# Performance work log

Measured on AMD Instinct MI355X. Metric: run time of the kernel, lower is better.

## Reference

```python
import jax, jax.numpy as jnp
import numpy as np

B, N, D = 32, 2048, 128
SQRT_DIM = np.sqrt(float(D)).astype(np.float32)  # scale=True -> 1/sqrt(dim)
MASK_FILL = -65504.0  # value used by masked_fill_ in the torch module


def setup_inputs() -> dict:
    key = jax.random.key(0)
    kq, kk, kv = jax.random.split(key, 3)
    return {
        "query": jax.random.normal(kq, (B, N, D), dtype=jnp.float32),
        "key": jax.random.normal(kk, (B, N, D), dtype=jnp.float32),
        "value": jax.random.normal(kv, (B, N, D), dtype=jnp.float32),
        "mask": jnp.ones((B, N, N), dtype=bool),
    }


def reference(query, key, value, mask):
    # score = Q K^T / sqrt(d)   -> [B, N, N]
    score = jnp.einsum("bnd,bmd->bnm", query, key) / SQRT_DIM
    # masked_fill_(~mask, -65504)
    score = jnp.where(mask, score, MASK_FILL)
    attn = jax.nn.softmax(score, axis=-1)
    # context = attn @ V        -> [B, N, D]
    context = jnp.einsum("bnm,bmd->bnd", attn, value)
    return (context, attn)
```

## Files before the change

### kernel.cpp

```cpp
#include <hip/hip_runtime.h>
#include <stdint.h>

#define B_ 32
#define N_ 2048
#define D_ 128
#define TQ 16
#define NW 8
#define CPW (N_ / NW)
#define NT (CPW / 16)
#define SCALE 0.08838834764831845f
#define MASK_FILL -65504.0f

typedef __attribute__((ext_vector_type(8))) short short8;
typedef __attribute__((ext_vector_type(4))) float f32x4;
typedef __attribute__((ext_vector_type(4))) int i32x4;

static __device__ __forceinline__ short f2bf(float f) {
    unsigned u = __builtin_bit_cast(unsigned, f);
    u += 0x7FFFu + ((u >> 16) & 1u);
    return (short)(u >> 16);
}

__global__ __launch_bounds__(512, 4)
void attn_fused_kernel(const float* __restrict__ Q, const float* __restrict__ K,
                       const float* __restrict__ V, const int* __restrict__ mask,
                       float* __restrict__ attn, float* __restrict__ ctx) {
    extern __shared__ char smem[];
    char*  Pb   = smem;
    float* redm = (float*)(smem + TQ * N_ * 2);
    float* reds = redm + NW * TQ;

    int wg = blockIdx.x;
    wg = (wg & 7) * (4096 / 8) + (wg >> 3);
    const int b    = wg >> 7;
    const int row0 = (wg & 127) * TQ;

    const int tid  = threadIdx.x;
    const int w    = tid >> 6;
    const int lane = tid & 63;
    const int l16  = lane & 15;
    const int quad = lane >> 4;

    const size_t qkvbase = (size_t)b * N_ * D_;

    short8 qf[4];
    {
        const float* qp = Q + qkvbase + (size_t)(row0 + l16) * D_ + quad * 8;
        #pragma unroll
        for (int kt = 0; kt < 4; ++kt) {
            f32x4 x = *(const f32x4*)(qp + kt * 32);
            f32x4 y = *(const f32x4*)(qp + kt * 32 + 4);
            #pragma unroll
            for (int j = 0; j < 4; ++j) { qf[kt][j] = f2bf(x[j]); qf[kt][4 + j] = f2bf(y[j]); }
        }
    }

    const int* mrow = mask + ((size_t)b * N_ + row0 + l16) * N_ + w * CPW + quad * 4;
    f32x4 acc[NT];
    float mmax = -INFINITY;
    #pragma unroll
    for (int t = 0; t < NT; ++t) {
        const int c0 = w * CPW + t * 16;
        const float* kp = K + qkvbase + (size_t)(c0 + l16) * D_ + quad * 8;
        i32x4 mv = *(const i32x4*)(mrow + t * 16);
        f32x4 a = {0.f, 0.f, 0.f, 0.f};
        #pragma unroll
        for (int kt = 0; kt < 4; ++kt) {
            f32x4 x = *(const f32x4*)(kp + kt * 32);
            f32x4 y = *(const f32x4*)(kp + kt * 32 + 4);
            short8 kf;
            #pragma unroll
            for (int j = 0; j < 4; ++j) { kf[j] = f2bf(x[j]); kf[4 + j] = f2bf(y[j]); }
            a = __builtin_amdgcn_mfma_f32_16x16x32_bf16(kf, qf[kt], a, 0, 0, 0);
        }
        #pragma unroll
        for (int r = 0; r < 4; ++r) {
            float s = mv[r] ? a[r] * SCALE : MASK_FILL;
            a[r] = s;
            mmax = fmaxf(mmax, s);
        }
        acc[t] = a;
    }

    mmax = fmaxf(mmax, __shfl_xor(mmax, 16));
    mmax = fmaxf(mmax, __shfl_xor(mmax, 32));
    if (quad == 0) redm[w * TQ + l16] = mmax;
    __syncthreads();
    float m = redm[l16];
    #pragma unroll
    for (int w2 = 1; w2 < NW; ++w2) m = fmaxf(m, redm[w2 * TQ + l16]);

    float sum = 0.f;
    #pragma unroll
    for (int t = 0; t < NT; ++t) {
        #pragma unroll
        for (int r = 0; r < 4; ++r) {
            float e = __expf(acc[t][r] - m);
            acc[t][r] = e;
            sum += e;
        }
    }
    sum += __shfl_xor(sum, 16);
    sum += __shfl_xor(sum, 32);
    if (quad == 0) reds[w * TQ + l16] = sum;
    __syncthreads();
    float rsum = reds[l16];
    #pragma unroll
    for (int w2 = 1; w2 < NW; ++w2) rsum += reds[w2 * TQ + l16];
    const float inv = 1.f / rsum;

    float* arow = attn + ((size_t)b * N_ + row0 + l16) * N_ + w * CPW + quad * 4;
    const unsigned pbase = (unsigned)(l16 * (N_ * 2) + (w * CPW + quad * 4) * 2);
    const unsigned swz   = (unsigned)((l16 & 7) << 4);
    #pragma unroll
    for (int t = 0; t < NT; ++t) {
        f32x4 vout;
        #pragma unroll
        for (int r = 0; r < 4; ++r) vout[r] = acc[t][r] * inv;
        *(f32x4*)(arow + t * 16) = vout;
        unsigned lo = (unsigned)(unsigned short)f2bf(vout[0]) | ((unsigned)(unsigned short)f2bf(vout[1]) << 16);
        unsigned hi = (unsigned)(unsigned short)f2bf(vout[2]) | ((unsigned)(unsigned short)f2bf(vout[3]) << 16);
        *(unsigned long long*)(Pb + ((pbase + t * 32) ^ swz)) = ((unsigned long long)hi << 32) | lo;
    }
    __syncthreads();

    const int n0 = w * 16;
    f32x4 o = {0.f, 0.f, 0.f, 0.f};
    const unsigned prbase = (unsigned)(l16 * (N_ * 2) + quad * 16);
    const float* vcol = V + qkvbase + (size_t)(quad * 8) * D_ + n0 + l16;
    #pragma unroll 4
    for (int kk = 0; kk < N_; kk += 32) {
        short8 pf = *(const short8*)(Pb + ((prbase + kk * 2) ^ swz));
        short8 vf;
        #pragma unroll
        for (int j = 0; j < 8; ++j) vf[j] = f2bf(vcol[(size_t)(kk + j) * D_]);
        o = __builtin_amdgcn_mfma_f32_16x16x32_bf16(vf, pf, o, 0, 0, 0);
    }
    float* crow = ctx + ((size_t)b * N_ + row0 + l16) * D_ + n0 + quad * 4;
    *(f32x4*)crow = o;
}

extern "C" void kernel_launch(void* const* d_in, const int* in_sizes, int n_in,
                              void* d_out, int out_size, void* d_ws, size_t ws_size,
                              hipStream_t stream) {
    const float* Q    = (const float*)d_in[0];
    const float* K    = (const float*)d_in[1];
    const float* V    = (const float*)d_in[2];
    const int*   mask = (const int*)d_in[3];

    float* out  = (float*)d_out;
    float* ctx  = out;
    float* attn = out + (size_t)B_ * N_ * D_;

    dim3 grid(B_ * (N_ / TQ), 1, 1);
    dim3 block(512, 1, 1);
    const size_t lds = (size_t)TQ * N_ * 2 + 2 * NW * TQ * sizeof(float);

    attn_fused_kernel<<<grid, block, lds, stream>>>(Q, K, V, mask, attn, ctx);
}
```

Measured before the change: 1.527 ms.

## Pre-convert K to bf16 and V to transposed bf16 in workspace

Adds two pre-pass kernels that convert K to bf16 and write V as a transposed bf16 copy into the workspace. The fused attention kernel can then load ready-made bf16 fragments with contiguous vector loads instead of converting fp32 inside the kernel and gathering V with strided scalar loads. Other changes: nontemporal loads for the mask, nontemporal stores for attn and ctx, and two accumulators in the PV loop. The cost is two extra launches and extra workspace traffic, and it falls back to the old path when the workspace is too small.

```diff
diff --git a/kernel.cpp b/kernel.cpp
--- a/kernel.cpp
+++ b/kernel.cpp
@@ -14,6 +14,8 @@
 typedef __attribute__((ext_vector_type(8))) short short8;
 typedef __attribute__((ext_vector_type(4))) float f32x4;
 typedef __attribute__((ext_vector_type(4))) int i32x4;
+typedef __attribute__((ext_vector_type(4))) unsigned short ushort4_t;
+typedef unsigned short ushort_t;
 
 static __device__ __forceinline__ short f2bf(float f) {
     unsigned u = __builtin_bit_cast(unsigned, f);
@@ -21,9 +23,41 @@
     return (short)(u >> 16);
 }
 
+__global__ __launch_bounds__(256)
+void conv_bf16_kernel(const float* __restrict__ X, ushort_t* __restrict__ Y) {
+    const size_t i = ((size_t)blockIdx.x * 256 + threadIdx.x) * 8;
+    f32x4 a = *(const f32x4*)(X + i);
+    f32x4 c = *(const f32x4*)(X + i + 4);
+    short8 o;
+    #pragma unroll
+    for (int j = 0; j < 4; ++j) { o[j] = f2bf(a[j]); o[4 + j] = f2bf(c[j]); }
+    *(short8*)(Y + i) = o;
+}
+
+__global__ __launch_bounds__(256)
+void conv_vt_kernel(const float* __restrict__ V, ushort_t* __restrict__ Vt) {
+    __shared__ ushort_t t[32][34];
+    const int tid = threadIdx.x;
+    const int b = blockIdx.z, n0 = blockIdx.x * 32, d0 = blockIdx.y * 32;
+    {
+        const int r = tid >> 3, cg = (tid & 7) * 4;
+        f32x4 v = *(const f32x4*)(V + ((size_t)b * N_ + n0 + r) * D_ + d0 + cg);
+        #pragma unroll
+        for (int j = 0; j < 4; ++j) t[r][cg + j] = (ushort_t)f2bf(v[j]);
+    }
+    __syncthreads();
+    {
+        const int d = tid >> 3, ng = (tid & 7) * 4;
+        ushort4_t o = { t[ng][d], t[ng + 1][d], t[ng + 2][d], t[ng + 3][d] };
+        *(ushort4_t*)(Vt + ((size_t)b * D_ + d0 + d) * N_ + n0 + ng) = o;
+    }
+}
+
+template <int PRE>
 __global__ __launch_bounds__(512, 4)
 void attn_fused_kernel(const float* __restrict__ Q, const float* __restrict__ K,
-                       const float* __restrict__ V, const int* __restrict__ mask,
+                       const ushort_t* __restrict__ Kb, const float* __restrict__ V,
+                       const ushort_t* __restrict__ Vt, const int* __restrict__ mask,
                        float* __restrict__ attn, float* __restrict__ ctx) {
     extern __shared__ char smem[];
     char*  Pb   = smem;
@@ -61,17 +95,26 @@
     #pragma unroll
     for (int t = 0; t < NT; ++t) {
         const int c0 = w * CPW + t * 16;
-        const float* kp = K + qkvbase + (size_t)(c0 + l16) * D_ + quad * 8;
-        i32x4 mv = *(const i32x4*)(mrow + t * 16);
+        i32x4 mv = __builtin_nontemporal_load((const i32x4*)(mrow + t * 16));
         f32x4 a = {0.f, 0.f, 0.f, 0.f};
-        #pragma unroll
-        for (int kt = 0; kt < 4; ++kt) {
-            f32x4 x = *(const f32x4*)(kp + kt * 32);
-            f32x4 y = *(const f32x4*)(kp + kt * 32 + 4);
-            short8 kf;
-            #pragma unroll
-            for (int j = 0; j < 4; ++j) { kf[j] = f2bf(x[j]); kf[4 + j] = f2bf(y[j]); }
-            a = __builtin_amdgcn_mfma_f32_16x16x32_bf16(kf, qf[kt], a, 0, 0, 0);
+        if constexpr (PRE) {
+            const ushort_t* kp = Kb + qkvbase + (size_t)(c0 + l16) * D_ + quad * 8;
+            #pragma unroll
+            for (int kt = 0; kt < 4; ++kt) {
+                short8 kf = *(const short8*)(kp + kt * 32);
+                a = __builtin_amdgcn_mfma_f32_16x16x32_bf16(kf, qf[kt], a, 0, 0, 0);
+            }
+        } else {
+            const float* kp = K + qkvbase + (size_t)(c0 + l16) * D_ + quad * 8;
+            #pragma unroll
+            for (int kt = 0; kt < 4; ++kt) {
+                f32x4 x = *(const f32x4*)(kp + kt * 32);
+                f32x4 y = *(const f32x4*)(kp + kt * 32 + 4);
+                short8 kf;
+                #pragma unroll
+                for (int j = 0; j < 4; ++j) { kf[j] = f2bf(x[j]); kf[4 + j] = f2bf(y[j]); }
+                a = __builtin_amdgcn_mfma_f32_16x16x32_bf16(kf, qf[kt], a, 0, 0, 0);
+            }
         }
         #pragma unroll
         for (int r = 0; r < 4; ++r) {
@@ -117,7 +160,7 @@
         f32x4 vout;
         #pragma unroll
         for (int r = 0; r < 4; ++r) vout[r] = acc[t][r] * inv;
-        *(f32x4*)(arow + t * 16) = vout;
+        __builtin_nontemporal_store(vout, (f32x4*)(arow + t * 16));
         unsigned lo = (unsigned)(unsigned short)f2bf(vout[0]) | ((unsigned)(unsigned short)f2bf(vout[1]) << 16);
         unsigned hi = (unsigned)(unsigned short)f2bf(vout[2]) | ((unsigned)(unsigned short)f2bf(vout[3]) << 16);
         *(unsigned long long*)(Pb + ((pbase + t * 32) ^ swz)) = ((unsigned long long)hi << 32) | lo;
@@ -125,19 +168,39 @@
     __syncthreads();
 
     const int n0 = w * 16;
-    f32x4 o = {0.f, 0.f, 0.f, 0.f};
+    f32x4 o0 = {0.f, 0.f, 0.f, 0.f};
+    f32x4 o1 = {0.f, 0.f, 0.f, 0.f};
     const unsigned prbase = (unsigned)(l16 * (N_ * 2) + quad * 16);
-    const float* vcol = V + qkvbase + (size_t)(quad * 8) * D_ + n0 + l16;
-    #pragma unroll 4
-    for (int kk = 0; kk < N_; kk += 32) {
-        short8 pf = *(const short8*)(Pb + ((prbase + kk * 2) ^ swz));
-        short8 vf;
-        #pragma unroll
-        for (int j = 0; j < 8; ++j) vf[j] = f2bf(vcol[(size_t)(kk + j) * D_]);
-        o = __builtin_amdgcn_mfma_f32_16x16x32_bf16(vf, pf, o, 0, 0, 0);
-    }
+    if constexpr (PRE) {
+        const ushort_t* vrow = Vt + qkvbase + (size_t)(n0 + l16) * N_ + quad * 8;
+        #pragma unroll 2
+        for (int kk = 0; kk < N_; kk += 64) {
+            short8 pf0 = *(const short8*)(Pb + ((prbase + kk * 2) ^ swz));
+            short8 pf1 = *(const short8*)(Pb + ((prbase + kk * 2 + 64) ^ swz));
+            short8 vf0 = *(const short8*)(vrow + kk);
+            short8 vf1 = *(const short8*)(vrow + kk + 32);
+            o0 = __builtin_amdgcn_mfma_f32_16x16x32_bf16(vf0, pf0, o0, 0, 0, 0);
+            o1 = __builtin_amdgcn_mfma_f32_16x16x32_bf16(vf1, pf1, o1, 0, 0, 0);
+        }
+    } else {
+        const float* vcol = V + qkvbase + (size_t)(quad * 8) * D_ + n0 + l16;
+        #pragma unroll 2
+        for (int kk = 0; kk < N_; kk += 64) {
+            short8 pf0 = *(const short8*)(Pb + ((prbase + kk * 2) ^ swz));
+            short8 pf1 = *(const short8*)(Pb + ((prbase + kk * 2 + 64) ^ swz));
+            short8 vf0, vf1;
+            #pragma unroll
+            for (int j = 0; j < 8; ++j) {
+                vf0[j] = f2bf(vcol[(size_t)(kk + j) * D_]);
+                vf1[j] = f2bf(vcol[(size_t)(kk + 32 + j) * D_]);
+            }
+            o0 = __builtin_amdgcn_mfma_f32_16x16x32_bf16(vf0, pf0, o0, 0, 0, 0);
+            o1 = __builtin_amdgcn_mfma_f32_16x16x32_bf16(vf1, pf1, o1, 0, 0, 0);
+        }
+    }
+    f32x4 o = o0 + o1;
     float* crow = ctx + ((size_t)b * N_ + row0 + l16) * D_ + n0 + quad * 4;
-    *(f32x4*)crow = o;
+    __builtin_nontemporal_store(o, (f32x4*)crow);
 }
 
 extern "C" void kernel_launch(void* const* d_in, const int* in_sizes, int n_in,
@@ -156,5 +219,18 @@
     dim3 block(512, 1, 1);
     const size_t lds = (size_t)TQ * N_ * 2 + 2 * NW * TQ * sizeof(float);
 
-    attn_fused_kernel<<<grid, block, lds, stream>>>(Q, K, V, mask, attn, ctx);
-}
+    const size_t nel = (size_t)B_ * N_ * D_;
+    const size_t ws_need = nel * 2 * 2;
+
+    if (ws_size >= ws_need) {
+        ushort_t* Kb = (ushort_t*)d_ws;
+        ushort_t* Vt = Kb + nel;
+        conv_bf16_kernel<<<dim3((unsigned)(nel / 8 / 256)), dim3(256), 0, stream>>>(K, Kb);
+        conv_vt_kernel<<<dim3(N_ / 32, D_ / 32, B_), dim3(256), 0, stream>>>(V, Vt);
+        attn_fused_kernel<1><<<grid, block, lds, stream>>>(Q, K, Kb, V, Vt, mask, attn, ctx);
+    } else {
+        attn_fused_kernel<0><<<grid, block, lds, stream>>>(Q, K, (const ushort_t*)nullptr,
+                                                           V, (const ushort_t*)nullptr,
+                                                           mask, attn, ctx);
+    }
+}
```

Result: faster. 1.415 ms (-7.3%).
